# Kernel tuning notes

Measured on AMD Instinct MI355X. Metric: run time of the kernel, lower is better.

The kernel has to match this reference:

```python
import jax, jax.numpy as jnp
import numpy as np

B, IN, C, H, E = 8192, 768, 64, 64, 16  # batch, input_dim, n_concepts, hidden_dim, embedding_dim


def setup_inputs() -> dict:
    key = jax.random.key(0)
    ks = jax.random.split(key, 10)

    def w(k, shape, fan_in):
        return jax.random.normal(k, shape, jnp.float32) / np.float32(np.sqrt(fan_in))

    inp = {"x": jax.random.normal(ks[0], (B, IN), jnp.float32)}
    i = 1
    for pre, din, dout in (("pos", IN, E), ("neg", IN, E), ("cp", 2 * E, 1)):
        inp[pre + "_W1"] = w(ks[i], (C, din, H), din)
        inp[pre + "_b1"] = jnp.zeros((C, H), jnp.float32)
        inp[pre + "_W2"] = w(ks[i + 1], (C, H, H), H)
        inp[pre + "_b2"] = jnp.zeros((C, H), jnp.float32)
        inp[pre + "_W3"] = w(ks[i + 2], (C, H, dout), H)
        inp[pre + "_b3"] = jnp.zeros((C, dout), jnp.float32)
        i += 3
    return inp


def _bank(x, W1, b1, W2, b2, W3, b3):
    # x: [B, IN]; per-concept MLP batched over C via einsum -> [B, C, E]
    h = jax.nn.relu(jnp.einsum('bi,cih->bch', x, W1) + b1)
    h = jax.nn.relu(jnp.einsum('bch,cho->bco', h, W2) + b2)
    return jnp.einsum('bch,che->bce', h, W3) + b3


def reference(x, pos_W1, pos_b1, pos_W2, pos_b2, pos_W3, pos_b3,
              neg_W1, neg_b1, neg_W2, neg_b2, neg_W3, neg_b3,
              cp_W1, cp_b1, cp_W2, cp_b2, cp_W3, cp_b3):
    pos = _bank(x, pos_W1, pos_b1, pos_W2, pos_b2, pos_W3, pos_b3)  # [B,C,E]
    neg = _bank(x, neg_W1, neg_b1, neg_W2, neg_b2, neg_W3, neg_b3)  # [B,C,E]
    # torch cat([pos, neg], dim=1) on [B,E,C], then x[:,:,i] -> per-concept [B, 2E]
    xc = jnp.concatenate([pos, neg], axis=-1)  # [B,C,2E]
    h = jax.nn.relu(jnp.einsum('bci,cih->bch', xc, cp_W1) + cp_b1)
    h = jax.nn.relu(jnp.einsum('bch,cho->bco', h, cp_W2) + cp_b2)
    concepts = (jnp.einsum('bch,cho->bco', h, cp_W3) + cp_b3)[..., 0]  # [B,C]
    w = jnp.clip(concepts * 0.5 + 0.5, 0.0, 1.0)[:, :, None]  # gate in [0,1]
    emb = pos * w + neg * (1.0 - w)  # [B,C,E]
    # torch layout is [B,E,C] then .view(B,-1): transpose before flattening
    emb_flat = jnp.transpose(emb, (0, 2, 1)).reshape(x.shape[0], E * C)
    return emb_flat, concepts
```

## Files before the change

kernel.cpp:

```cpp
#include <hip/hip_runtime.h>
#include <hip/hip_bf16.h>


#define B_   8192
#define IN_  768
#define C_   64
#define H_   64
#define E_   16
#define BM_  128

typedef __bf16 bf16x8 __attribute__((ext_vector_type(8)));
typedef float  f32x4  __attribute__((ext_vector_type(4)));

__device__ __forceinline__ f32x4 mfma16(bf16x8 a, bf16x8 b, f32x4 c) {
  return __builtin_amdgcn_mfma_f32_16x16x32_bf16(a, b, c, 0, 0, 0);
}

__device__ __forceinline__ bf16x8 cvt8(float4 a, float4 b) {
  bf16x8 r;
  r[0] = (__bf16)a.x; r[1] = (__bf16)a.y; r[2] = (__bf16)a.z; r[3] = (__bf16)a.w;
  r[4] = (__bf16)b.x; r[5] = (__bf16)b.y; r[6] = (__bf16)b.z; r[7] = (__bf16)b.w;
  return r;
}

__device__ __forceinline__ void gll16(const __bf16* g, __bf16* l) {
  __builtin_amdgcn_global_load_lds(
      (const __attribute__((address_space(1))) unsigned int*)g,
      (__attribute__((address_space(3))) unsigned int*)l, 16, 0, 0);
}

struct __align__(16) SmemT {
  __bf16 xs[2 * 128 * 64];
  __bf16 wbuf[2 * 128 * 64];
};
static_assert(sizeof(SmemT) == 65536, "layout");
static_assert(sizeof(SmemT) <= 81920, "LDS: need 2 blocks/CU");

template <int MT>
__device__ __forceinline__ void epi64s(__bf16* hb, f32x4 (&acc)[MT][4],
                                       const float* __restrict__ bias,
                                       int rb, int quad, int l16) {
#pragma unroll
  for (int nt = 0; nt < 4; ++nt) {
    const int ch = nt * 2 + (l16 >> 3);
    const int cl = l16 & 7;
    const float bv = bias[nt * 16 + l16];
#pragma unroll
    for (int mt = 0; mt < MT; ++mt)
#pragma unroll
      for (int r = 0; r < 4; ++r) {
        const int row = rb + mt * 16 + quad * 4 + r;
        hb[row * 64 + (((ch ^ (row & 7)) << 3) | cl)] =
            (__bf16)fmaxf(acc[mt][nt][r] + bv, 0.f);
      }
  }
}

__global__ __launch_bounds__(256, 2) void cb_fused_t(
    const __bf16* __restrict__ x,
    const __bf16* __restrict__ pW1t, const float* __restrict__ pb1,
    const __bf16* __restrict__ pW2t, const float* __restrict__ pb2,
    const __bf16* __restrict__ pW3t, const float* __restrict__ pb3,
    const __bf16* __restrict__ nW1t, const float* __restrict__ nb1,
    const __bf16* __restrict__ nW2t, const float* __restrict__ nb2,
    const __bf16* __restrict__ nW3t, const float* __restrict__ nb3,
    const __bf16* __restrict__ cW1t, const float* __restrict__ cb1,
    const __bf16* __restrict__ cW2t, const float* __restrict__ cb2,
    const __bf16* __restrict__ cw3,  const float* __restrict__ cb3,
    float* __restrict__ out_emb, float* __restrict__ out_con)
{
  __shared__ SmemT sm;
  const int tid  = threadIdx.x;
  const int wave = tid >> 6, lane = tid & 63;
  const int quad = lane >> 4, l16 = lane & 15;
  const int bank = wave >> 1;
  const int rb   = (wave & 1) * 64;
  const int s7   = l16 & 7;
  const int row0 = blockIdx.x * BM_;
  const int c    = blockIdx.y;

  const __bf16* pg = pW1t + (size_t)c * 64 * IN_;
  const __bf16* ng = nW1t + (size_t)c * 64 * IN_;

  f32x4 acc[4][4];
  {
    const f32x4 z = {0.f, 0.f, 0.f, 0.f};
#pragma unroll
    for (int mt = 0; mt < 4; ++mt)
#pragma unroll
      for (int nt = 0; nt < 4; ++nt) acc[mt][nt] = z;
  }

  const __bf16* xg = x + (size_t)row0 * IN_;
  const int lrow = lane >> 3;
  const int lchunk = (lane & 7) ^ lrow;
  const __bf16* xsrc = xg + (size_t)(wave * 32 + lrow) * IN_ + lchunk * 8;
  const __bf16* wgsrc = (wave < 2)
      ? pg + (size_t)(wave * 32 + lrow) * IN_ + lchunk * 8
      : ng + (size_t)((wave - 2) * 32 + lrow) * IN_ + lchunk * 8;
  const int wdrow = (wave < 2) ? wave * 32 : 64 + (wave - 2) * 32;

#pragma unroll
  for (int j = 0; j < 4; ++j)
    gll16(xsrc + j * 8 * IN_, sm.xs + (wave * 32 + j * 8) * 64);
#pragma unroll
  for (int j = 0; j < 4; ++j)
    gll16(wgsrc + j * 8 * IN_, sm.wbuf + (wdrow + j * 8) * 64);
  __builtin_amdgcn_sched_barrier(0);

  for (int kt = 0; kt < 12; ++kt) {
    if (kt < 11) {
      const int ko = (kt + 1) * 64;
      __bf16* xd = sm.xs   + ((kt + 1) & 1) * 8192;
      __bf16* wd = sm.wbuf + ((kt + 1) & 1) * 8192;
#pragma unroll
      for (int j = 0; j < 4; ++j)
        gll16(xsrc + j * 8 * IN_ + ko, xd + (wave * 32 + j * 8) * 64);
#pragma unroll
      for (int j = 0; j < 4; ++j)
        gll16(wgsrc + j * 8 * IN_ + ko, wd + (wdrow + j * 8) * 64);
      asm volatile("s_waitcnt vmcnt(8)" ::: "memory");
    } else {
      asm volatile("s_waitcnt vmcnt(0)" ::: "memory");
    }
    __builtin_amdgcn_s_barrier();
    __builtin_amdgcn_sched_barrier(0);
    const __bf16* xb = sm.xs   + (kt & 1) * 8192;
    const __bf16* wb = sm.wbuf + (kt & 1) * 8192 + bank * 4096;
#pragma unroll
    for (int ks = 0; ks < 2; ++ks) {
      const int pc = ((ks * 4 + quad) ^ s7) << 3;
      bf16x8 a[4], bb[4];
#pragma unroll
      for (int mt = 0; mt < 4; ++mt)
        a[mt] = *(const bf16x8*)(xb + (rb + mt * 16 + l16) * 64 + pc);
#pragma unroll
      for (int nt = 0; nt < 4; ++nt)
        bb[nt] = *(const bf16x8*)(wb + (nt * 16 + l16) * 64 + pc);
#pragma unroll
      for (int mt = 0; mt < 4; ++mt)
#pragma unroll
        for (int nt = 0; nt < 4; ++nt)
          acc[mt][nt] = mfma16(a[mt], bb[nt], acc[mt][nt]);
    }
    __builtin_amdgcn_sched_barrier(0);
    __builtin_amdgcn_s_barrier();
    __builtin_amdgcn_sched_barrier(0);
  }
  __syncthreads();

  __bf16* hbP  = sm.wbuf;
  __bf16* hbN  = sm.wbuf + 8192;
  __bf16* hbX  = bank ? hbN : hbP;
  __bf16* xcb  = sm.xs;
  float*  conc = (float*)(sm.xs + 5120);

  const __bf16* W2g = (bank ? nW2t : pW2t) + (size_t)c * 4096;
  const __bf16* W3g = (bank ? nW3t : pW3t) + (size_t)c * 1024;
  const float*  b1c = (bank ? nb1 : pb1) + c * 64;
  const float*  b2c = (bank ? nb2 : pb2) + c * 64;
  const float*  b3c = (bank ? nb3 : pb3) + c * 16;

  bf16x8 bb2[2][4];
#pragma unroll
  for (int ks = 0; ks < 2; ++ks)
#pragma unroll
    for (int nt = 0; nt < 4; ++nt)
      bb2[ks][nt] = *(const bf16x8*)(W2g + (nt * 16 + l16) * 64 + ks * 32 + quad * 8);

  epi64s<4>(hbX, acc, b1c, rb, quad, l16);

  f32x4 acc2[4][4];
  {
    const f32x4 z = {0.f, 0.f, 0.f, 0.f};
#pragma unroll
    for (int mt = 0; mt < 4; ++mt)
#pragma unroll
      for (int nt = 0; nt < 4; ++nt) acc2[mt][nt] = z;
  }
#pragma unroll
  for (int ks = 0; ks < 2; ++ks) {
    const int off = ((ks * 4 + quad) ^ s7) << 3;
    bf16x8 a[4];
#pragma unroll
    for (int mt = 0; mt < 4; ++mt)
      a[mt] = *(const bf16x8*)(hbX + (rb + mt * 16 + l16) * 64 + off);
#pragma unroll
    for (int mt = 0; mt < 4; ++mt)
#pragma unroll
      for (int nt = 0; nt < 4; ++nt)
        acc2[mt][nt] = mfma16(a[mt], bb2[ks][nt], acc2[mt][nt]);
  }

  bf16x8 bb3[2];
#pragma unroll
  for (int ks = 0; ks < 2; ++ks)
    bb3[ks] = *(const bf16x8*)(W3g + l16 * 64 + ks * 32 + quad * 8);

  epi64s<4>(hbX, acc2, b2c, rb, quad, l16);

  {
    f32x4 acc3[4];
    const f32x4 z = {0.f, 0.f, 0.f, 0.f};
#pragma unroll
    for (int mt = 0; mt < 4; ++mt) acc3[mt] = z;
#pragma unroll
    for (int ks = 0; ks < 2; ++ks) {
      const int off = ((ks * 4 + quad) ^ s7) << 3;
#pragma unroll
      for (int mt = 0; mt < 4; ++mt) {
        bf16x8 a = *(const bf16x8*)(hbX + (rb + mt * 16 + l16) * 64 + off);
        acc3[mt] = mfma16(a, bb3[ks], acc3[mt]);
      }
    }
    const float bv = b3c[l16];
#pragma unroll
    for (int mt = 0; mt < 4; ++mt)
#pragma unroll
      for (int r = 0; r < 4; ++r) {
        const int row = rb + mt * 16 + quad * 4 + r;
        xcb[row * 40 + bank * 16 + l16] = (__bf16)(acc3[mt][r] + bv);
      }
  }
  __syncthreads();

  const int r2 = wave * 32;
  {
    const __bf16* c1 = cW1t + (size_t)c * 2048;
    bf16x8 bc1[4];
#pragma unroll
    for (int nt = 0; nt < 4; ++nt)
      bc1[nt] = *(const bf16x8*)(c1 + (nt * 16 + l16) * 32 + quad * 8);
    f32x4 acc1[2][4];
    {
      const f32x4 z = {0.f, 0.f, 0.f, 0.f};
#pragma unroll
      for (int mt = 0; mt < 2; ++mt)
#pragma unroll
        for (int nt = 0; nt < 4; ++nt) acc1[mt][nt] = z;
    }
    bf16x8 a1[2];
#pragma unroll
    for (int mt = 0; mt < 2; ++mt)
      a1[mt] = *(const bf16x8*)&xcb[(r2 + mt * 16 + l16) * 40 + quad * 8];
#pragma unroll
    for (int mt = 0; mt < 2; ++mt)
#pragma unroll
      for (int nt = 0; nt < 4; ++nt)
        acc1[mt][nt] = mfma16(a1[mt], bc1[nt], acc1[mt][nt]);

    const __bf16* c2 = cW2t + (size_t)c * 4096;
    bf16x8 bc2[2][4];
#pragma unroll
    for (int ks = 0; ks < 2; ++ks)
#pragma unroll
      for (int nt = 0; nt < 4; ++nt)
        bc2[ks][nt] = *(const bf16x8*)(c2 + (nt * 16 + l16) * 64 + ks * 32 + quad * 8);

    epi64s<2>(hbP, acc1, cb1 + c * 64, r2, quad, l16);

    f32x4 accC[2][4];
    {
      const f32x4 z = {0.f, 0.f, 0.f, 0.f};
#pragma unroll
      for (int mt = 0; mt < 2; ++mt)
#pragma unroll
        for (int nt = 0; nt < 4; ++nt) accC[mt][nt] = z;
    }
#pragma unroll
    for (int ks = 0; ks < 2; ++ks) {
      const int off = ((ks * 4 + quad) ^ s7) << 3;
      bf16x8 a[2];
#pragma unroll
      for (int mt = 0; mt < 2; ++mt)
        a[mt] = *(const bf16x8*)(hbP + (r2 + mt * 16 + l16) * 64 + off);
#pragma unroll
      for (int mt = 0; mt < 2; ++mt)
#pragma unroll
        for (int nt = 0; nt < 4; ++nt)
          accC[mt][nt] = mfma16(a[mt], bc2[ks][nt], accC[mt][nt]);
    }
    epi64s<2>(hbP, accC, cb2 + c * 64, r2, quad, l16);

    f32x4 acc3b[2];
    {
      const f32x4 z = {0.f, 0.f, 0.f, 0.f};
      acc3b[0] = z; acc3b[1] = z;
    }
#pragma unroll
    for (int ks = 0; ks < 2; ++ks) {
      const int off = ((ks * 4 + quad) ^ s7) << 3;
      bf16x8 bbv = {};
      if (l16 == 0) bbv = *(const bf16x8*)(cw3 + (size_t)c * 64 + ks * 32 + quad * 8);
#pragma unroll
      for (int mt = 0; mt < 2; ++mt) {
        bf16x8 a = *(const bf16x8*)(hbP + (r2 + mt * 16 + l16) * 64 + off);
        acc3b[mt] = mfma16(a, bbv, acc3b[mt]);
      }
    }
    if (l16 == 0) {
      float bv = cb3[c];
#pragma unroll
      for (int mt = 0; mt < 2; ++mt)
#pragma unroll
        for (int r = 0; r < 4; ++r)
          conc[r2 + mt * 16 + quad * 4 + r] = acc3b[mt][r] + bv;
    }
  }
  __syncthreads();

  for (int ii = tid; ii < BM_ * E_; ii += 256) {
    int row = ii >> 4, e = ii & 15;
    float cv = conc[row];
    float w  = fminf(fmaxf(cv * 0.5f + 0.5f, 0.f), 1.f);
    float pv2 = (float)xcb[row * 40 + e];
    float nv2 = (float)xcb[row * 40 + 16 + e];
    out_emb[(size_t)(row0 + row) * (E_ * C_) + e * C_ + c] = pv2 * w + nv2 * (1.f - w);
  }
  if (tid < 128) out_con[(size_t)(row0 + tid) * C_ + c] = conc[tid];
}

#define TSEG 5
#define PSEG 5
struct PrepArgs {
  const float* tsrc[TSEG];
  __bf16*      tdst[TSEG];
  int tstart[TSEG + 1];
  int ktiles[TSEG];
  const float* psrc[PSEG];
  __bf16*      pdst[PSEG];
  int pstart[PSEG + 1];
  int pchunks[PSEG];
  int kdiv8[PSEG];
  int N[PSEG];
  int tblocks;
};

__global__ __launch_bounds__(256) void prep_all(PrepArgs a) {
  const int tid = threadIdx.x;
  const int b = blockIdx.x;
  __shared__ __bf16 lt[64 * 72];
  if (b < a.tblocks) {
    int s = 0;
    while (s < TSEG - 1 && b >= a.tstart[s + 1]) ++s;
    const int idx = b - a.tstart[s];
    const int kt = idx % a.ktiles[s];
    const int c  = idx / a.ktiles[s];
    const int K  = a.ktiles[s] * 64;
    const float* src = a.tsrc[s] + (size_t)c * K * 64 + (size_t)kt * 64 * 64;
    __bf16*      dst = a.tdst[s] + (size_t)c * 64 * K + kt * 64;
    const int r = tid >> 4, c4 = (tid & 15) * 4;
#pragma unroll
    for (int it = 0; it < 4; ++it) {
      int k = r + it * 16;
      float4 v = *(const float4*)(src + (size_t)k * 64 + c4);
      lt[(c4 + 0) * 72 + k] = (__bf16)v.x;
      lt[(c4 + 1) * 72 + k] = (__bf16)v.y;
      lt[(c4 + 2) * 72 + k] = (__bf16)v.z;
      lt[(c4 + 3) * 72 + k] = (__bf16)v.w;
    }
    __syncthreads();
    const int n = tid >> 3, i = tid & 7;
#pragma unroll
    for (int it = 0; it < 2; ++it) {
      int nn = n + it * 32;
      *(uint4*)(dst + (size_t)nn * K + i * 8) = *(const uint4*)&lt[nn * 72 + i * 8];
    }
  } else {
    const int bb = b - a.tblocks;
    int s = 0;
    while (s < PSEG - 1 && bb >= a.pstart[s + 1]) ++s;
    const int lb  = bb - a.pstart[s];
    const int nch = a.pchunks[s];
    const int kc  = a.kdiv8[s];
    const int N   = a.N[s];
#pragma unroll
    for (int j = 0; j < 4; ++j) {
      const int li = (lb * 4 + j) * 256 + tid;
      if (li >= nch) break;
      if (N == 1) {
        const float4* src = (const float4*)a.psrc[s] + (size_t)li * 2;
        float4 v0 = src[0], v1 = src[1];
        *(uint4*)(a.pdst[s] + (size_t)li * 8) = __builtin_bit_cast(uint4, cvt8(v0, v1));
      } else {
        int rn = li / kc;
        int k0 = (li - rn * kc) * 8;
        int cc = rn / N;
        int n  = rn - cc * N;
        const float* src = a.psrc[s] + ((size_t)cc * kc * 8 + k0) * N + n;
        bf16x8 r;
#pragma unroll
        for (int jj = 0; jj < 8; ++jj) r[jj] = (__bf16)src[(size_t)jj * N];
        *(uint4*)(a.pdst[s] + (size_t)rn * kc * 8 + k0) = __builtin_bit_cast(uint4, r);
      }
    }
  }
}

extern "C" void kernel_launch(void* const* d_in, const int* in_sizes, int n_in,
                              void* d_out, int out_size, void* d_ws, size_t ws_size,
                              hipStream_t stream) {
  const float* xf   = (const float*)d_in[0];
  const float* pW1f = (const float*)d_in[1];
  const float* pb1f = (const float*)d_in[2];
  const float* pW2f = (const float*)d_in[3];
  const float* pb2f = (const float*)d_in[4];
  const float* pW3f = (const float*)d_in[5];
  const float* pb3f = (const float*)d_in[6];
  const float* nW1f = (const float*)d_in[7];
  const float* nb1f = (const float*)d_in[8];
  const float* nW2f = (const float*)d_in[9];
  const float* nb2f = (const float*)d_in[10];
  const float* nW3f = (const float*)d_in[11];
  const float* nb3f = (const float*)d_in[12];
  const float* cW1f = (const float*)d_in[13];
  const float* cb1f = (const float*)d_in[14];
  const float* cW2f = (const float*)d_in[15];
  const float* cb2f = (const float*)d_in[16];
  const float* cW3f = (const float*)d_in[17];
  const float* cb3f = (const float*)d_in[18];

  float* out_emb = (float*)d_out;
  float* out_con = out_emb + (size_t)B_ * E_ * C_;

  const int cx   = B_ * IN_;
  const int cW1c = C_ * IN_ * H_;
  const int cW2c = C_ * H_ * H_;
  const int cW3c = C_ * H_ * E_;
  const int ccW1 = C_ * 2 * E_ * H_;
  const int ccW3 = C_ * H_;

  __bf16* w = (__bf16*)d_ws;
  size_t o = 0;
  __bf16* xw   = w + o; o += cx;
  __bf16* pw1t = w + o; o += cW1c;
  __bf16* nw1t = w + o; o += cW1c;
  __bf16* pw2t = w + o; o += cW2c;
  __bf16* nw2t = w + o; o += cW2c;
  __bf16* cw2t = w + o; o += cW2c;
  __bf16* pw3t = w + o; o += cW3c;
  __bf16* nw3t = w + o; o += cW3c;
  __bf16* cw1t = w + o; o += ccW1;
  __bf16* cw3w = w + o; o += ccW3;

  PrepArgs a;
  int tb = 0, pb = 0;
  {
    const float* tsrc[TSEG] = {pW1f, nW1f, pW2f, nW2f, cW2f};
    __bf16*      tdst[TSEG] = {pw1t, nw1t, pw2t, nw2t, cw2t};
    const int    tk[TSEG]   = {12,   12,   1,    1,    1};
    for (int i = 0; i < TSEG; ++i) {
      a.tsrc[i] = tsrc[i]; a.tdst[i] = tdst[i]; a.ktiles[i] = tk[i];
      a.tstart[i] = tb;
      tb += tk[i] * C_;
    }
    a.tstart[TSEG] = tb;
    a.tblocks = tb;

    const float* psrc[PSEG] = {xf, cW3f, pW3f, nW3f, cW1f};
    __bf16*      pdst[PSEG] = {xw, cw3w, pw3t, nw3t, cw1t};
    const int    pKs[PSEG]  = {0,  0,    64,   64,   32};
    const int    pNs[PSEG]  = {1,  1,    16,   16,   64};
    const int    pels[PSEG] = {cx, ccW3, cW3c, cW3c, ccW1};
    for (int i = 0; i < PSEG; ++i) {
      a.psrc[i] = psrc[i]; a.pdst[i] = pdst[i];
      a.pchunks[i] = pels[i] / 8;
      a.kdiv8[i] = (pNs[i] == 1) ? (pels[i] / 8) : (pKs[i] / 8);
      a.N[i] = pNs[i];
      a.pstart[i] = pb;
      pb += (pels[i] / 8 + 1023) / 1024;
    }
    a.pstart[PSEG] = pb;
  }
  prep_all<<<tb + pb, 256, 0, stream>>>(a);

  dim3 grid(B_ / BM_, C_);
  cb_fused_t<<<grid, 256, 0, stream>>>(xw,
      pw1t, pb1f, pw2t, pb2f, pw3t, pb3f,
      nw1t, nb1f, nw2t, nb2f, nw3t, nb3f,
      cw1t, cb1f, cw2t, cb2f, cw3w, cb3f,
      out_emb, out_con);
}
```

Before: 315.0 us.

## Triple-buffer layer-1 weight tiles and prefetch tail weights into LDS

```diff
diff --git a/kernel.cpp b/kernel.cpp
--- a/kernel.cpp
+++ b/kernel.cpp
@@ -29,12 +29,17 @@
       (__attribute__((address_space(3))) unsigned int*)l, 16, 0, 0);
 }
 
+__device__ __forceinline__ void gll_w64(const __bf16* M, __bf16* dst, int rbase, int lane) {
+  const int lr = lane >> 3, lc = (lane & 7) ^ lr;
+  gll16(M + (size_t)(rbase + lr) * 64 + lc * 8, dst + rbase * 64);
+}
+
 struct __align__(16) SmemT {
-  __bf16 xs[2 * 128 * 64];
-  __bf16 wbuf[2 * 128 * 64];
+  __bf16 xs[2][8192];
+  __bf16 wb[2][8192];
+  __bf16 wt[8192];
 };
-static_assert(sizeof(SmemT) == 65536, "layout");
-static_assert(sizeof(SmemT) <= 81920, "LDS: need 2 blocks/CU");
+static_assert(sizeof(SmemT) == 81920, "layout");
 
 template <int MT>
 __device__ __forceinline__ void epi64s(__bf16* hb, f32x4 (&acc)[MT][4],
@@ -102,31 +107,62 @@
 
 #pragma unroll
   for (int j = 0; j < 4; ++j)
-    gll16(xsrc + j * 8 * IN_, sm.xs + (wave * 32 + j * 8) * 64);
+    gll16(wgsrc + j * 8 * IN_, sm.wb[0] + (wdrow + j * 8) * 64);
 #pragma unroll
   for (int j = 0; j < 4; ++j)
-    gll16(wgsrc + j * 8 * IN_, sm.wbuf + (wdrow + j * 8) * 64);
+    gll16(xsrc + j * 8 * IN_, sm.xs[0] + (wave * 32 + j * 8) * 64);
+#pragma unroll
+  for (int j = 0; j < 4; ++j)
+    gll16(wgsrc + j * 8 * IN_ + 64, sm.wb[1] + (wdrow + j * 8) * 64);
   __builtin_amdgcn_sched_barrier(0);
 
+#pragma unroll
   for (int kt = 0; kt < 12; ++kt) {
-    if (kt < 11) {
-      const int ko = (kt + 1) * 64;
-      __bf16* xd = sm.xs   + ((kt + 1) & 1) * 8192;
-      __bf16* wd = sm.wbuf + ((kt + 1) & 1) * 8192;
+    if (kt < 10) {
+      __bf16* xd = sm.xs[(kt + 1) & 1];
 #pragma unroll
       for (int j = 0; j < 4; ++j)
-        gll16(xsrc + j * 8 * IN_ + ko, xd + (wave * 32 + j * 8) * 64);
+        gll16(xsrc + j * 8 * IN_ + (kt + 1) * 64, xd + (wave * 32 + j * 8) * 64);
+      __bf16* wd = ((kt + 2) % 3 == 0) ? sm.wb[0]
+                 : ((kt + 2) % 3 == 1) ? sm.wb[1] : sm.wt;
 #pragma unroll
       for (int j = 0; j < 4; ++j)
-        gll16(wgsrc + j * 8 * IN_ + ko, wd + (wdrow + j * 8) * 64);
+        gll16(wgsrc + j * 8 * IN_ + (kt + 2) * 64, wd + (wdrow + j * 8) * 64);
+      asm volatile("s_waitcnt vmcnt(12)" ::: "memory");
+    } else if (kt == 10) {
+#pragma unroll
+      for (int j = 0; j < 4; ++j)
+        gll16(xsrc + j * 8 * IN_ + 11 * 64, sm.xs[1] + (wave * 32 + j * 8) * 64);
       asm volatile("s_waitcnt vmcnt(8)" ::: "memory");
     } else {
-      asm volatile("s_waitcnt vmcnt(0)" ::: "memory");
+      if (wave == 0) {
+        const __bf16* M = pW2t + (size_t)c * 4096;
+#pragma unroll
+        for (int g = 0; g < 8; ++g) gll_w64(M, sm.wb[0], g * 8, lane);
+        asm volatile("s_waitcnt vmcnt(8)" ::: "memory");
+      } else if (wave == 1) {
+        const __bf16* M = nW2t + (size_t)c * 4096;
+#pragma unroll
+        for (int g = 0; g < 8; ++g) gll_w64(M, sm.wb[0] + 4096, g * 8, lane);
+        asm volatile("s_waitcnt vmcnt(8)" ::: "memory");
+      } else if (wave == 2) {
+        const __bf16* m3p = pW3t + (size_t)c * 1024;
+        const __bf16* m3n = nW3t + (size_t)c * 1024;
+        gll_w64(m3p, sm.wb[1], 0, lane);
+        gll_w64(m3p, sm.wb[1], 8, lane);
+        gll_w64(m3n, sm.wb[1] + 1024, 0, lane);
+        gll_w64(m3n, sm.wb[1] + 1024, 8, lane);
+        asm volatile("s_waitcnt vmcnt(4)" ::: "memory");
+      } else {
+        if (lane < 8) gll16(cw3 + (size_t)c * 64 + lane * 8, sm.wb[1] + 2048);
+        asm volatile("s_waitcnt vmcnt(1)" ::: "memory");
+      }
     }
     __builtin_amdgcn_s_barrier();
     __builtin_amdgcn_sched_barrier(0);
-    const __bf16* xb = sm.xs   + (kt & 1) * 8192;
-    const __bf16* wb = sm.wbuf + (kt & 1) * 8192 + bank * 4096;
+    const __bf16* xb = sm.xs[kt & 1];
+    const __bf16* wbp = ((kt % 3 == 0) ? sm.wb[0]
+                       : (kt % 3 == 1) ? sm.wb[1] : sm.wt) + bank * 4096;
 #pragma unroll
     for (int ks = 0; ks < 2; ++ks) {
       const int pc = ((ks * 4 + quad) ^ s7) << 3;
@@ -136,7 +172,7 @@
         a[mt] = *(const bf16x8*)(xb + (rb + mt * 16 + l16) * 64 + pc);
 #pragma unroll
       for (int nt = 0; nt < 4; ++nt)
-        bb[nt] = *(const bf16x8*)(wb + (nt * 16 + l16) * 64 + pc);
+        bb[nt] = *(const bf16x8*)(wbp + (nt * 16 + l16) * 64 + pc);
 #pragma unroll
       for (int mt = 0; mt < 4; ++mt)
 #pragma unroll
@@ -149,24 +185,32 @@
   }
   __syncthreads();
 
-  __bf16* hbP  = sm.wbuf;
-  __bf16* hbN  = sm.wbuf + 8192;
+  __bf16* hbP  = sm.xs[0];
+  __bf16* hbN  = sm.xs[1];
   __bf16* hbX  = bank ? hbN : hbP;
-  __bf16* xcb  = sm.xs;
-  float*  conc = (float*)(sm.xs + 5120);
-
-  const __bf16* W2g = (bank ? nW2t : pW2t) + (size_t)c * 4096;
-  const __bf16* W3g = (bank ? nW3t : pW3t) + (size_t)c * 1024;
+  __bf16* xcb  = sm.wt;
+  float*  conc = (float*)(sm.wt + 5120);
+  const __bf16* W2l = sm.wb[0] + bank * 4096;
+  const __bf16* W3l = sm.wb[1] + bank * 1024;
+  const __bf16* cw3l = sm.wb[1] + 2048;
   const float*  b1c = (bank ? nb1 : pb1) + c * 64;
   const float*  b2c = (bank ? nb2 : pb2) + c * 64;
   const float*  b3c = (bank ? nb3 : pb3) + c * 16;
 
-  bf16x8 bb2[2][4];
-#pragma unroll
-  for (int ks = 0; ks < 2; ++ks)
+  bf16x8 bc1[4], bc2[2][4];
+  {
+    const __bf16* c1 = cW1t + (size_t)c * 2048;
+    const __bf16* c2 = cW2t + (size_t)c * 4096;
 #pragma unroll
     for (int nt = 0; nt < 4; ++nt)
-      bb2[ks][nt] = *(const bf16x8*)(W2g + (nt * 16 + l16) * 64 + ks * 32 + quad * 8);
+      bc1[nt] = *(const bf16x8*)(c1 + (nt * 16 + l16) * 32 + quad * 8);
+#pragma unroll
+    for (int ks = 0; ks < 2; ++ks)
+#pragma unroll
+      for (int nt = 0; nt < 4; ++nt)
+        bc2[ks][nt] = *(const bf16x8*)(c2 + (nt * 16 + l16) * 64 + ks * 32 + quad * 8);
+  }
+  __builtin_amdgcn_sched_barrier(0);
 
   epi64s<4>(hbX, acc, b1c, rb, quad, l16);
 
@@ -181,22 +225,19 @@
 #pragma unroll
   for (int ks = 0; ks < 2; ++ks) {
     const int off = ((ks * 4 + quad) ^ s7) << 3;
-    bf16x8 a[4];
+    bf16x8 a[4], bb[4];
 #pragma unroll
     for (int mt = 0; mt < 4; ++mt)
       a[mt] = *(const bf16x8*)(hbX + (rb + mt * 16 + l16) * 64 + off);
 #pragma unroll
+    for (int nt = 0; nt < 4; ++nt)
+      bb[nt] = *(const bf16x8*)(W2l + (nt * 16 + l16) * 64 + off);
+#pragma unroll
     for (int mt = 0; mt < 4; ++mt)
 #pragma unroll
       for (int nt = 0; nt < 4; ++nt)
-        acc2[mt][nt] = mfma16(a[mt], bb2[ks][nt], acc2[mt][nt]);
-  }
-
-  bf16x8 bb3[2];
-#pragma unroll
-  for (int ks = 0; ks < 2; ++ks)
-    bb3[ks] = *(const bf16x8*)(W3g + l16 * 64 + ks * 32 + quad * 8);
-
+        acc2[mt][nt] = mfma16(a[mt], bb[nt], acc2[mt][nt]);
+  }
   epi64s<4>(hbX, acc2, b2c, rb, quad, l16);
 
   {
@@ -207,10 +248,11 @@
 #pragma unroll
     for (int ks = 0; ks < 2; ++ks) {
       const int off = ((ks * 4 + quad) ^ s7) << 3;
+      bf16x8 bb = *(const bf16x8*)(W3l + l16 * 64 + off);
 #pragma unroll
       for (int mt = 0; mt < 4; ++mt) {
         bf16x8 a = *(const bf16x8*)(hbX + (rb + mt * 16 + l16) * 64 + off);
-        acc3[mt] = mfma16(a, bb3[ks], acc3[mt]);
+        acc3[mt] = mfma16(a, bb, acc3[mt]);
       }
     }
     const float bv = b3c[l16];
@@ -226,11 +268,6 @@
 
   const int r2 = wave * 32;
   {
-    const __bf16* c1 = cW1t + (size_t)c * 2048;
-    bf16x8 bc1[4];
-#pragma unroll
-    for (int nt = 0; nt < 4; ++nt)
-      bc1[nt] = *(const bf16x8*)(c1 + (nt * 16 + l16) * 32 + quad * 8);
     f32x4 acc1[2][4];
     {
       const f32x4 z = {0.f, 0.f, 0.f, 0.f};
@@ -248,15 +285,6 @@
 #pragma unroll
       for (int nt = 0; nt < 4; ++nt)
         acc1[mt][nt] = mfma16(a1[mt], bc1[nt], acc1[mt][nt]);
-
-    const __bf16* c2 = cW2t + (size_t)c * 4096;
-    bf16x8 bc2[2][4];
-#pragma unroll
-    for (int ks = 0; ks < 2; ++ks)
-#pragma unroll
-      for (int nt = 0; nt < 4; ++nt)
-        bc2[ks][nt] = *(const bf16x8*)(c2 + (nt * 16 + l16) * 64 + ks * 32 + quad * 8);
-
     epi64s<2>(hbP, acc1, cb1 + c * 64, r2, quad, l16);
 
     f32x4 accC[2][4];
@@ -291,7 +319,7 @@
     for (int ks = 0; ks < 2; ++ks) {
       const int off = ((ks * 4 + quad) ^ s7) << 3;
       bf16x8 bbv = {};
-      if (l16 == 0) bbv = *(const bf16x8*)(cw3 + (size_t)c * 64 + ks * 32 + quad * 8);
+      if (l16 == 0) bbv = *(const bf16x8*)(cw3l + ks * 32 + quad * 8);
 #pragma unroll
       for (int mt = 0; mt < 2; ++mt) {
         bf16x8 a = *(const bf16x8*)(hbP + (r2 + mt * 16 + l16) * 64 + off);
```

New measurement: 315.1 us. About the same (+0.0%).
